# Kernel optimization log

Measured on AMD Instinct MI355X. Metric: run time of the kernel, lower is better.

The kernel has to match this reference:

```python
import jax, jax.numpy as jnp
import numpy as np

B, S, H = 2, 1024, 4096
NH, NKV, D = 32, 8, 128
N_REP = NH // NKV
SCALE = D ** -0.5
ROPE_BASE = 1000000.0
NEG_INF = -1e9


def _rope_tables(dtype=jnp.float32):
    inv_freq = 1.0 / (ROPE_BASE ** (jnp.arange(0, D, 2, dtype=jnp.float32) / D))
    pos = jnp.arange(S, dtype=jnp.float32)
    freqs = pos[:, None] * inv_freq[None, :]              # [S, D/2]
    emb = jnp.concatenate([freqs, freqs], axis=-1)        # [S, D]
    cos = jnp.broadcast_to(jnp.cos(emb)[None], (B, S, D)).astype(dtype)
    sin = jnp.broadcast_to(jnp.sin(emb)[None], (B, S, D)).astype(dtype)
    return cos, sin


def setup_inputs() -> dict:
    key = jax.random.key(0)
    k1, k2, k3, k4, k5 = jax.random.split(key, 5)
    hidden_states = jax.random.normal(k1, (B, S, H), dtype=jnp.float32)
    # weights stored as [in, out] so application is x @ W
    Wq = jax.random.normal(k2, (H, NH * D), dtype=jnp.float32) * (H ** -0.5)
    Wk = jax.random.normal(k3, (H, NKV * D), dtype=jnp.float32) * (H ** -0.5)
    Wv = jax.random.normal(k4, (H, NKV * D), dtype=jnp.float32) * (H ** -0.5)
    Wo = jax.random.normal(k5, (NH * D, H), dtype=jnp.float32) * ((NH * D) ** -0.5)
    cos, sin = _rope_tables()
    causal = jnp.tril(jnp.ones((S, S), dtype=bool))
    attention_mask = jnp.where(causal, 0.0, NEG_INF).astype(jnp.float32)
    attention_mask = jnp.broadcast_to(attention_mask[None, None], (B, 1, S, S))
    return {"hidden_states": hidden_states, "cos": cos, "sin": sin,
            "attention_mask": attention_mask, "Wq": Wq, "Wk": Wk, "Wv": Wv, "Wo": Wo}


def _rotate_half(x):
    x1, x2 = x[..., : D // 2], x[..., D // 2:]
    return jnp.concatenate([-x2, x1], axis=-1)


def reference(hidden_states, cos, sin, attention_mask, Wq, Wk, Wv, Wo):
    # projections -> [B, heads, S, D]
    q = (hidden_states @ Wq).reshape(B, S, NH, D).transpose(0, 2, 1, 3)
    k = (hidden_states @ Wk).reshape(B, S, NKV, D).transpose(0, 2, 1, 3)
    v = (hidden_states @ Wv).reshape(B, S, NKV, D).transpose(0, 2, 1, 3)
    # RoPE (cos/sin unsqueezed over head dim)
    c = cos[:, None, :, :]
    s = sin[:, None, :, :]
    q = q * c + _rotate_half(q) * s
    k = k * c + _rotate_half(k) * s
    # repeat_kv for GQA
    k = jnp.repeat(k, N_REP, axis=1)   # [B, NH, S, D]
    v = jnp.repeat(v, N_REP, axis=1)
    scores = jnp.einsum('bhqd,bhkd->bhqk', q, k) * SCALE + attention_mask
    weights = jax.nn.softmax(scores.astype(jnp.float32), axis=-1).astype(q.dtype)
    attn = jnp.einsum('bhqk,bhkd->bhqd', weights, v)
    attn = attn.transpose(0, 2, 1, 3).reshape(B, S, NH * D)
    return attn @ Wo
```

## Files before the change

kernel.cpp:

```cpp
#include <hip/hip_runtime.h>

typedef unsigned short u16;
typedef __bf16 bf16x8 __attribute__((ext_vector_type(8)));
typedef float f32x4 __attribute__((ext_vector_type(4)));

#define SCALE_QK 0.08838834764831845f
#define LOG2E 1.4426950408889634f
#define NEGBIG (-1e9f)

static __device__ __forceinline__ float bf2f(u16 u) {
  union { float f; unsigned int i; } x; x.i = ((unsigned int)u) << 16; return x.f;
}
static __device__ __forceinline__ u16 f2bf(float f) {
  union { float f; unsigned int i; } x; x.f = f;
  return (u16)((x.i + 0x7fffu + ((x.i >> 16) & 1u)) >> 16);
}
static __device__ __forceinline__ void async16(const u16* g, u16* s) {
  __builtin_amdgcn_global_load_lds(
      (const __attribute__((address_space(1))) void*)g,
      (__attribute__((address_space(3))) void*)s, 16, 0, 0);
}

__global__ __launch_bounds__(64) void detect_dtype(
    const void* p0, const void* p1, const void* p2, const void* p3,
    const void* p4, const void* p5, int* flags) {
  const void* ps[6] = {p0, p1, p2, p3, p4, p5};
  const u16* p = (const u16*)ps[blockIdx.x];
  int lane = threadIdx.x;
  u16 u = p[2 * lane];
  int e = (u >> 7) & 0xFF;
  int plaus = (e >= 112 && e <= 143) ? 1 : 0;
  unsigned long long m = __ballot(plaus);
  if (lane == 0) {
    flags[blockIdx.x] = (__popcll(m) < 32) ? 1 : 0;
    if (blockIdx.x == 0) flags[6] = 0;
  }
}

__global__ __launch_bounds__(256) void transpose_to_bf16(
    const void* __restrict__ src, u16* __restrict__ dst, int N, int K,
    const int* __restrict__ flag) {
  const int LT = 74;
  __shared__ u16 t[64 * LT];
  const int tid = threadIdx.x;
  const int n0 = blockIdx.x * 64, k0 = blockIdx.y * 64;
  const int f32in = *flag;
  for (int c = tid; c < 512; c += 256) {
    int r = c >> 3, ch = (c & 7) * 8;
    u16* tp = t + r * LT + ch;
    if (f32in) {
      const float* p = (const float*)src + (size_t)(k0 + r) * N + n0 + ch;
      float4 v0 = *(const float4*)p;
      float4 v1 = *(const float4*)(p + 4);
      tp[0] = f2bf(v0.x); tp[1] = f2bf(v0.y); tp[2] = f2bf(v0.z); tp[3] = f2bf(v0.w);
      tp[4] = f2bf(v1.x); tp[5] = f2bf(v1.y); tp[6] = f2bf(v1.z); tp[7] = f2bf(v1.w);
    } else {
      uint4 v = *(const uint4*)((const u16*)src + (size_t)(k0 + r) * N + n0 + ch);
      const u16* pv = (const u16*)&v;
#pragma unroll
      for (int e = 0; e < 8; ++e) tp[e] = pv[e];
    }
  }
  __syncthreads();
  for (int c = tid; c < 512; c += 256) {
    int rr = c >> 3, cc = (c & 7) * 8;
    u16 tmp[8];
#pragma unroll
    for (int e = 0; e < 8; ++e) tmp[e] = t[(cc + e) * LT + rr];
    *(uint4*)(dst + (size_t)(n0 + rr) * K + k0 + cc) = *(const uint4*)tmp;
  }
}

__global__ __launch_bounds__(256) void cast_to_bf16(
    const void* __restrict__ src, u16* __restrict__ dst, const int* __restrict__ flag) {
  int i = (blockIdx.x * 256 + threadIdx.x) * 8;
  if (*flag) {
    float4 v0 = *(const float4*)((const float*)src + i);
    float4 v1 = *(const float4*)((const float*)src + i + 4);
    u16 tmp[8] = {f2bf(v0.x), f2bf(v0.y), f2bf(v0.z), f2bf(v0.w),
                  f2bf(v1.x), f2bf(v1.y), f2bf(v1.z), f2bf(v1.w)};
    *(uint4*)(dst + i) = *(const uint4*)tmp;
  } else {
    *(uint4*)(dst + i) = *(const uint4*)((const u16*)src + i);
  }
}

__global__ __launch_bounds__(256, 2) void gemm_bt(
    const u16* __restrict__ A, const u16* __restrict__ Bt, void* __restrict__ C,
    int K, int lda, int ldb, int ldc, const int* __restrict__ oflag) {
  __shared__ u16 sA[128 * 32];
  __shared__ u16 sB[128 * 32];
  const int tid = threadIdx.x;
  const int wave = tid >> 6, lane = tid & 63;
  const int quad = lane >> 4, l16 = lane & 15;
  const int wr = wave >> 1, wc = wave & 1;
  const int bm = blockIdx.y << 7, bn = blockIdx.x << 7;
  const int f32out = *oflag;

  f32x4 acc[4][4] = {};

  const int c0 = tid, c1 = tid + 256;
  const int r0 = c0 >> 2, h0 = (c0 & 3) * 8;
  const int r1 = c1 >> 2, h1 = (c1 & 3) * 8;
  const u16* a0 = A + (size_t)(bm + r0) * lda + h0;
  const u16* a1 = A + (size_t)(bm + r1) * lda + h1;
  const u16* b0 = Bt + (size_t)(bn + r0) * ldb + h0;
  const u16* b1 = Bt + (size_t)(bn + r1) * ldb + h1;

  for (int k0 = 0; k0 < K; k0 += 32) {
    async16(a0 + k0, sA + c0 * 8);
    async16(a1 + k0, sA + c1 * 8);
    async16(b0 + k0, sB + c0 * 8);
    async16(b1 + k0, sB + c1 * 8);
    __syncthreads();
    bf16x8 af[4], bv[4];
#pragma unroll
    for (int i = 0; i < 4; ++i)
      af[i] = *(const bf16x8*)(sA + (wr * 64 + i * 16 + l16) * 32 + quad * 8);
#pragma unroll
    for (int j = 0; j < 4; ++j)
      bv[j] = *(const bf16x8*)(sB + (wc * 64 + j * 16 + l16) * 32 + quad * 8);
#pragma unroll
    for (int i = 0; i < 4; ++i)
#pragma unroll
      for (int j = 0; j < 4; ++j)
        acc[i][j] =
            __builtin_amdgcn_mfma_f32_16x16x32_bf16(af[i], bv[j], acc[i][j], 0, 0, 0);
    __syncthreads();
  }
#pragma unroll
  for (int i = 0; i < 4; ++i) {
    int row = bm + wr * 64 + i * 16 + quad * 4;
#pragma unroll
    for (int j = 0; j < 4; ++j) {
      int col = bn + wc * 64 + j * 16 + l16;
#pragma unroll
      for (int r = 0; r < 4; ++r) {
        size_t idx = (size_t)(row + r) * ldc + col;
        if (f32out) ((float*)C)[idx] = acc[i][j][r];
        else ((u16*)C)[idx] = f2bf(acc[i][j][r]);
      }
    }
  }
}

__global__ __launch_bounds__(256) void rope_kernel(
    u16* __restrict__ QKV, const void* __restrict__ cosb,
    const void* __restrict__ sinb, const int* __restrict__ flag) {
  int idx = blockIdx.x * 256 + threadIdx.x;
  int d = idx & 63;
  int rest = idx >> 6;
  int slot = rest % 40;
  int tok = rest / 40;
  int col = (slot < 32) ? (slot * 128 + d) : (4096 + (slot - 32) * 128 + d);
  size_t base = (size_t)tok * 6144 + col;
  float x1 = bf2f(QKV[base]);
  float x2 = bf2f(QKV[base + 64]);
  size_t cb = (size_t)tok * 128 + d;
  float c1, s1, c2, s2;
  if (*flag) {
    c1 = ((const float*)cosb)[cb]; s1 = ((const float*)sinb)[cb];
    c2 = ((const float*)cosb)[cb + 64]; s2 = ((const float*)sinb)[cb + 64];
  } else {
    c1 = bf2f(((const u16*)cosb)[cb]); s1 = bf2f(((const u16*)sinb)[cb]);
    c2 = bf2f(((const u16*)cosb)[cb + 64]); s2 = bf2f(((const u16*)sinb)[cb + 64]);
  }
  QKV[base] = f2bf(x1 * c1 - x2 * s1);
  QKV[base + 64] = f2bf(x2 * c2 + x1 * s2);
}

__global__ __launch_bounds__(256, 3) void attn_kernel(
    const u16* __restrict__ QKV, u16* __restrict__ O) {
  const int LK = 136;
  const int LP = 72;
  __shared__ u16 sK[64 * LK];
  __shared__ u16 sV[128 * 64];
  __shared__ u16 sP[64 * LP];
  const int tid = threadIdx.x, wave = tid >> 6, lane = tid & 63;
  const int quad = lane >> 4, l16 = lane & 15;
  const int pp = blockIdx.x, h = blockIdx.y, b = blockIdx.z;
  const int kvh = h >> 2;
  const size_t tb = (size_t)b * 1024 * 6144;
  const u16* Qg = QKV + tb + (size_t)h * 128;
  const u16* Kg = QKV + tb + 4096 + (size_t)kvh * 128;
  const u16* Vg = QKV + tb + 5120 + (size_t)kvh * 128;

#pragma unroll 1
  for (int pass = 0; pass < 2; ++pass) {
    const int qt = pass ? (15 - pp) : pp;

    bf16x8 qa[4];
    {
      const int qrow = qt * 64 + wave * 16 + l16;
#pragma unroll
      for (int kc = 0; kc < 4; ++kc) {
        bf16x8 v = *(const bf16x8*)(Qg + (size_t)qrow * 6144 + kc * 32 + quad * 8);
#pragma unroll
        for (int e = 0; e < 8; ++e) v[e] = (__bf16)((float)v[e] * (SCALE_QK * LOG2E));
        qa[kc] = v;
      }
    }

    uint4 kreg[4], vreg[4];
#pragma unroll
    for (int i = 0; i < 4; ++i) {
      int c = i * 256 + tid, row = c >> 4, ch = (c & 15) * 8;
      kreg[i] = *(const uint4*)(Kg + (size_t)row * 6144 + ch);
      vreg[i] = *(const uint4*)(Vg + (size_t)row * 6144 + ch);
    }

    float m_run[4], l_run[4];
    f32x4 oacc[8] = {};
#pragma unroll
    for (int r = 0; r < 4; ++r) { m_run[r] = -INFINITY; l_run[r] = 0.f; }

    const int nkb = qt + 1;
    for (int kb = 0; kb < nkb; ++kb) {
#pragma unroll
      for (int i = 0; i < 4; ++i) {
        int c = i * 256 + tid, row = c >> 4, ch = (c & 15) * 8;
        *(uint4*)(sK + row * LK + ch) = kreg[i];
        const u16* pw = (const u16*)&vreg[i];
#pragma unroll
        for (int e = 0; e < 8; ++e) {
          int d = ch + e;
          sV[d * 64 + ((((row >> 3) ^ (d >> 3)) & 7) << 3) + (row & 7)] = pw[e];
        }
      }
      __syncthreads();
      if (kb + 1 < nkb) {
#pragma unroll
        for (int i = 0; i < 4; ++i) {
          int c = i * 256 + tid, row = c >> 4, ch = (c & 15) * 8;
          kreg[i] = *(const uint4*)(Kg + (size_t)((kb + 1) * 64 + row) * 6144 + ch);
          vreg[i] = *(const uint4*)(Vg + (size_t)((kb + 1) * 64 + row) * 6144 + ch);
        }
      }

      f32x4 sc[4] = {};
#pragma unroll
      for (int kc = 0; kc < 4; ++kc)
#pragma unroll
        for (int j = 0; j < 4; ++j) {
          bf16x8 bb = *(const bf16x8*)(sK + (j * 16 + l16) * LK + kc * 32 + quad * 8);
          sc[j] = __builtin_amdgcn_mfma_f32_16x16x32_bf16(qa[kc], bb, sc[j], 0, 0, 0);
        }

      const int rowg = qt * 64 + wave * 16 + quad * 4;
      const int colg = kb * 64 + l16;
      float mloc[4] = {NEGBIG, NEGBIG, NEGBIG, NEGBIG};
#pragma unroll
      for (int j = 0; j < 4; ++j)
#pragma unroll
        for (int r = 0; r < 4; ++r) {
          float v = sc[j][r];
          if (colg + j * 16 > rowg + r) v = NEGBIG;
          sc[j][r] = v;
          mloc[r] = fmaxf(mloc[r], v);
        }
#pragma unroll
      for (int off = 1; off < 16; off <<= 1)
#pragma unroll
        for (int r = 0; r < 4; ++r)
          mloc[r] = fmaxf(mloc[r], __shfl_xor(mloc[r], off, 64));

      float alpha[4], lad[4];
#pragma unroll
      for (int r = 0; r < 4; ++r) {
        float mn = fmaxf(m_run[r], mloc[r]);
        alpha[r] = exp2f(m_run[r] - mn);
        m_run[r] = mn;
        lad[r] = 0.f;
      }
#pragma unroll
      for (int j = 0; j < 4; ++j)
#pragma unroll
        for (int r = 0; r < 4; ++r) {
          float p = exp2f(sc[j][r] - m_run[r]);
          sc[j][r] = p;
          lad[r] += p;
        }
#pragma unroll
      for (int off = 1; off < 16; off <<= 1)
#pragma unroll
        for (int r = 0; r < 4; ++r) lad[r] += __shfl_xor(lad[r], off, 64);
#pragma unroll
      for (int r = 0; r < 4; ++r) l_run[r] = l_run[r] * alpha[r] + lad[r];
#pragma unroll
      for (int dt = 0; dt < 8; ++dt)
#pragma unroll
        for (int r = 0; r < 4; ++r) oacc[dt][r] *= alpha[r];

#pragma unroll
      for (int j = 0; j < 4; ++j)
#pragma unroll
        for (int r = 0; r < 4; ++r)
          sP[(wave * 16 + quad * 4 + r) * LP + j * 16 + l16] = f2bf(sc[j][r]);
      __asm__ __volatile__("s_waitcnt lgkmcnt(0)" ::: "memory");

#pragma unroll
      for (int kc = 0; kc < 2; ++kc) {
        bf16x8 a = *(const bf16x8*)(sP + (wave * 16 + l16) * LP + kc * 32 + quad * 8);
#pragma unroll
        for (int dt = 0; dt < 8; ++dt) {
          int d = dt * 16 + l16;
          int chk = ((kc * 4 + quad) ^ (d >> 3)) & 7;
          bf16x8 bb = *(const bf16x8*)(sV + d * 64 + chk * 8);
          oacc[dt] = __builtin_amdgcn_mfma_f32_16x16x32_bf16(a, bb, oacc[dt], 0, 0, 0);
        }
      }
      __syncthreads();
    }

    const int srow = qt * 64 + wave * 16 + quad * 4;
#pragma unroll
    for (int dt = 0; dt < 8; ++dt)
#pragma unroll
      for (int r = 0; r < 4; ++r) {
        float val = oacc[dt][r] / l_run[r];
        O[((size_t)b * 1024 + srow + r) * 4096 + h * 128 + dt * 16 + l16] = f2bf(val);
      }
  }
}

extern "C" void kernel_launch(void* const* d_in, const int* in_sizes, int n_in,
                              void* d_out, int out_size, void* d_ws, size_t ws_size,
                              hipStream_t stream) {
  (void)in_sizes; (void)n_in; (void)out_size; (void)ws_size;
  const void* hidden = d_in[0];
  const void* cosb   = d_in[1];
  const void* sinb   = d_in[2];
  const void* Wq = d_in[4];
  const void* Wk = d_in[5];
  const void* Wv = d_in[6];
  const void* Wo = d_in[7];

  u16* ws = (u16*)d_ws;
  u16* Wqkvt = ws;
  u16* Wot   = ws;
  u16* Xb    = ws + (size_t)25165824;
  u16* attnb = Xb;
  u16* QKV   = ws + (size_t)33554432;
  int* flags = (int*)(ws + (size_t)46137344);

  detect_dtype<<<6, 64, 0, stream>>>(hidden, cosb, Wq, Wk, Wv, Wo, flags);

  transpose_to_bf16<<<dim3(64, 64), 256, 0, stream>>>(Wq, Wqkvt, 4096, 4096, flags + 2);
  transpose_to_bf16<<<dim3(16, 64), 256, 0, stream>>>(Wk, Wqkvt + (size_t)4096 * 4096, 1024, 4096, flags + 3);
  transpose_to_bf16<<<dim3(16, 64), 256, 0, stream>>>(Wv, Wqkvt + (size_t)5120 * 4096, 1024, 4096, flags + 4);
  cast_to_bf16<<<4096, 256, 0, stream>>>(hidden, Xb, flags + 0);

  gemm_bt<<<dim3(48, 16), 256, 0, stream>>>(Xb, Wqkvt, QKV, 4096, 4096, 4096, 6144, flags + 6);
  rope_kernel<<<20480, 256, 0, stream>>>(QKV, cosb, sinb, flags + 1);

  transpose_to_bf16<<<dim3(64, 64), 256, 0, stream>>>(Wo, Wot, 4096, 4096, flags + 5);

  attn_kernel<<<dim3(8, 32, 2), 256, 0, stream>>>(QKV, attnb);
  gemm_bt<<<dim3(32, 16), 256, 0, stream>>>(attnb, Wot, d_out, 4096, 4096, 4096, 4096, flags + 0);
}
```

Measured before the change: 519.7 us.

## Merge QKV transposes, vectorize RoPE, transpose attention scores with lazy rescaling

Folds the three Q/K/V weight transposes into one launch and rewrites RoPE so each thread handles eight contiguous elements with 16-byte loads and stores. In attention, the QK^T MFMA operands are swapped so each lane owns a single query row. That cuts the row max/sum reductions to two shuffles and keeps running stats in scalars, and the output rescale is skipped unless the max grows by more than 8 (log2 domain). The lazy rescale leaves exponent sums less tightly bounded, and the strided sP writes may add LDS bank conflicts.

```diff
diff --git a/kernel.cpp b/kernel.cpp
--- a/kernel.cpp
+++ b/kernel.cpp
@@ -37,14 +37,11 @@
   }
 }
 
-__global__ __launch_bounds__(256) void transpose_to_bf16(
+static __device__ __forceinline__ void transpose_body(
     const void* __restrict__ src, u16* __restrict__ dst, int N, int K,
-    const int* __restrict__ flag) {
+    int n0, int k0, int f32in, u16* t) {
   const int LT = 74;
-  __shared__ u16 t[64 * LT];
   const int tid = threadIdx.x;
-  const int n0 = blockIdx.x * 64, k0 = blockIdx.y * 64;
-  const int f32in = *flag;
   for (int c = tid; c < 512; c += 256) {
     int r = c >> 3, ch = (c & 7) * 8;
     u16* tp = t + r * LT + ch;
@@ -71,6 +68,26 @@
   }
 }
 
+__global__ __launch_bounds__(256) void transpose_to_bf16(
+    const void* __restrict__ src, u16* __restrict__ dst, int N, int K,
+    const int* __restrict__ flag) {
+  __shared__ u16 t[64 * 74];
+  transpose_body(src, dst, N, K, blockIdx.x * 64, blockIdx.y * 64, *flag, t);
+}
+
+__global__ __launch_bounds__(256) void transpose_qkv(
+    const void* __restrict__ Wq, const void* __restrict__ Wk,
+    const void* __restrict__ Wv, u16* __restrict__ dst,
+    const int* __restrict__ flags) {
+  __shared__ u16 t[64 * 74];
+  int bx = blockIdx.x;
+  const void* src; u16* d; int N; int f32in; int nx;
+  if (bx < 64)      { src = Wq; d = dst;                         N = 4096; f32in = flags[2]; nx = bx; }
+  else if (bx < 80) { src = Wk; d = dst + (size_t)4096 * 4096;   N = 1024; f32in = flags[3]; nx = bx - 64; }
+  else              { src = Wv; d = dst + (size_t)5120 * 4096;   N = 1024; f32in = flags[4]; nx = bx - 80; }
+  transpose_body(src, d, N, 4096, nx * 64, blockIdx.y * 64, f32in, t);
+}
+
 __global__ __launch_bounds__(256) void cast_to_bf16(
     const void* __restrict__ src, u16* __restrict__ dst, const int* __restrict__ flag) {
   int i = (blockIdx.x * 256 + threadIdx.x) * 8;
@@ -148,25 +165,53 @@
     u16* __restrict__ QKV, const void* __restrict__ cosb,
     const void* __restrict__ sinb, const int* __restrict__ flag) {
   int idx = blockIdx.x * 256 + threadIdx.x;
-  int d = idx & 63;
-  int rest = idx >> 6;
+  int d8 = (idx & 7) * 8;
+  int rest = idx >> 3;
   int slot = rest % 40;
   int tok = rest / 40;
-  int col = (slot < 32) ? (slot * 128 + d) : (4096 + (slot - 32) * 128 + d);
+  int col = (slot < 32) ? (slot * 128 + d8) : (4096 + (slot - 32) * 128 + d8);
   size_t base = (size_t)tok * 6144 + col;
-  float x1 = bf2f(QKV[base]);
-  float x2 = bf2f(QKV[base + 64]);
-  size_t cb = (size_t)tok * 128 + d;
-  float c1, s1, c2, s2;
+  uint4 va = *(const uint4*)(QKV + base);
+  uint4 vb = *(const uint4*)(QKV + base + 64);
+  const u16* pa = (const u16*)&va;
+  const u16* pb = (const u16*)&vb;
+  size_t cb = (size_t)tok * 128 + d8;
+  float c1[8], s1[8], c2[8], s2[8];
   if (*flag) {
-    c1 = ((const float*)cosb)[cb]; s1 = ((const float*)sinb)[cb];
-    c2 = ((const float*)cosb)[cb + 64]; s2 = ((const float*)sinb)[cb + 64];
+    const float* cp = (const float*)cosb + cb;
+    const float* sp = (const float*)sinb + cb;
+    float4 t0 = *(const float4*)cp,        t1 = *(const float4*)(cp + 4);
+    float4 t2 = *(const float4*)(cp + 64), t3 = *(const float4*)(cp + 68);
+    float4 u0 = *(const float4*)sp,        u1 = *(const float4*)(sp + 4);
+    float4 u2 = *(const float4*)(sp + 64), u3 = *(const float4*)(sp + 68);
+    const float* tf = (const float*)&t0;
+    (void)tf;
+    c1[0]=t0.x;c1[1]=t0.y;c1[2]=t0.z;c1[3]=t0.w;c1[4]=t1.x;c1[5]=t1.y;c1[6]=t1.z;c1[7]=t1.w;
+    c2[0]=t2.x;c2[1]=t2.y;c2[2]=t2.z;c2[3]=t2.w;c2[4]=t3.x;c2[5]=t3.y;c2[6]=t3.z;c2[7]=t3.w;
+    s1[0]=u0.x;s1[1]=u0.y;s1[2]=u0.z;s1[3]=u0.w;s1[4]=u1.x;s1[5]=u1.y;s1[6]=u1.z;s1[7]=u1.w;
+    s2[0]=u2.x;s2[1]=u2.y;s2[2]=u2.z;s2[3]=u2.w;s2[4]=u3.x;s2[5]=u3.y;s2[6]=u3.z;s2[7]=u3.w;
   } else {
-    c1 = bf2f(((const u16*)cosb)[cb]); s1 = bf2f(((const u16*)sinb)[cb]);
-    c2 = bf2f(((const u16*)cosb)[cb + 64]); s2 = bf2f(((const u16*)sinb)[cb + 64]);
-  }
-  QKV[base] = f2bf(x1 * c1 - x2 * s1);
-  QKV[base + 64] = f2bf(x2 * c2 + x1 * s2);
+    const u16* cp = (const u16*)cosb + cb;
+    const u16* sp = (const u16*)sinb + cb;
+    uint4 t0 = *(const uint4*)cp, t1 = *(const uint4*)(cp + 64);
+    uint4 u0 = *(const uint4*)sp, u1 = *(const uint4*)(sp + 64);
+    const u16* q0 = (const u16*)&t0; const u16* q1 = (const u16*)&t1;
+    const u16* r0 = (const u16*)&u0; const u16* r1 = (const u16*)&u1;
+#pragma unroll
+    for (int e = 0; e < 8; ++e) {
+      c1[e] = bf2f(q0[e]); c2[e] = bf2f(q1[e]);
+      s1[e] = bf2f(r0[e]); s2[e] = bf2f(r1[e]);
+    }
+  }
+  u16 o1[8], o2[8];
+#pragma unroll
+  for (int e = 0; e < 8; ++e) {
+    float x1 = bf2f(pa[e]), x2 = bf2f(pb[e]);
+    o1[e] = f2bf(x1 * c1[e] - x2 * s1[e]);
+    o2[e] = f2bf(x2 * c2[e] + x1 * s2[e]);
+  }
+  *(uint4*)(QKV + base) = *(const uint4*)o1;
+  *(uint4*)(QKV + base + 64) = *(const uint4*)o2;
 }
 
 __global__ __launch_bounds__(256, 3) void attn_kernel(
@@ -209,10 +254,9 @@
       vreg[i] = *(const uint4*)(Vg + (size_t)row * 6144 + ch);
     }
 
-    float m_run[4], l_run[4];
+    float m_run = -INFINITY, l_run = 0.f;
     f32x4 oacc[8] = {};
-#pragma unroll
-    for (int r = 0; r < 4; ++r) { m_run[r] = -INFINITY; l_run[r] = 0.f; }
+    const int qg = qt * 64 + wave * 16 + l16;
 
     const int nkb = qt + 1;
     for (int kb = 0; kb < nkb; ++kb) {
@@ -237,65 +281,61 @@
         }
       }
 
-      f32x4 sc[4] = {};
+      f32x4 st[4] = {};
 #pragma unroll
       for (int kc = 0; kc < 4; ++kc)
 #pragma unroll
         for (int j = 0; j < 4; ++j) {
           bf16x8 bb = *(const bf16x8*)(sK + (j * 16 + l16) * LK + kc * 32 + quad * 8);
-          sc[j] = __builtin_amdgcn_mfma_f32_16x16x32_bf16(qa[kc], bb, sc[j], 0, 0, 0);
-        }
-
-      const int rowg = qt * 64 + wave * 16 + quad * 4;
-      const int colg = kb * 64 + l16;
-      float mloc[4] = {NEGBIG, NEGBIG, NEGBIG, NEGBIG};
+          st[j] = __builtin_amdgcn_mfma_f32_16x16x32_bf16(bb, qa[kc], st[j], 0, 0, 0);
+        }
+
+      const int kg0 = kb * 64 + quad * 4;
+      float mloc = NEGBIG;
 #pragma unroll
       for (int j = 0; j < 4; ++j)
 #pragma unroll
         for (int r = 0; r < 4; ++r) {
-          float v = sc[j][r];
-          if (colg + j * 16 > rowg + r) v = NEGBIG;
-          sc[j][r] = v;
-          mloc[r] = fmaxf(mloc[r], v);
-        }
-#pragma unroll
-      for (int off = 1; off < 16; off <<= 1)
+          float v = st[j][r];
+          if (kg0 + j * 16 + r > qg) v = NEGBIG;
+          st[j][r] = v;
+          mloc = fmaxf(mloc, v);
+        }
+      mloc = fmaxf(mloc, __shfl_xor(mloc, 16, 64));
+      mloc = fmaxf(mloc, __shfl_xor(mloc, 32, 64));
+
+      if (__any(mloc - m_run > 8.0f)) {
+        float mn = fmaxf(m_run, mloc);
+        float alpha = exp2f(m_run - mn);
+        m_run = mn;
+        l_run *= alpha;
+        float ar[4];
+#pragma unroll
+        for (int r = 0; r < 4; ++r) ar[r] = __shfl(alpha, quad * 4 + r, 64);
+#pragma unroll
+        for (int dt = 0; dt < 8; ++dt)
+#pragma unroll
+          for (int r = 0; r < 4; ++r) oacc[dt][r] *= ar[r];
+      }
+
+      float lad = 0.f;
+#pragma unroll
+      for (int j = 0; j < 4; ++j)
+#pragma unroll
+        for (int r = 0; r < 4; ++r) {
+          float p = exp2f(st[j][r] - m_run);
+          st[j][r] = p;
+          lad += p;
+        }
+      lad += __shfl_xor(lad, 16, 64);
+      lad += __shfl_xor(lad, 32, 64);
+      l_run += lad;
+
+#pragma unroll
+      for (int j = 0; j < 4; ++j)
 #pragma unroll
         for (int r = 0; r < 4; ++r)
-          mloc[r] = fmaxf(mloc[r], __shfl_xor(mloc[r], off, 64));
-
-      float alpha[4], lad[4];
-#pragma unroll
-      for (int r = 0; r < 4; ++r) {
-        float mn = fmaxf(m_run[r], mloc[r]);
-        alpha[r] = exp2f(m_run[r] - mn);
-        m_run[r] = mn;
-        lad[r] = 0.f;
-      }
-#pragma unroll
-      for (int j = 0; j < 4; ++j)
-#pragma unroll
-        for (int r = 0; r < 4; ++r) {
-          float p = exp2f(sc[j][r] - m_run[r]);
-          sc[j][r] = p;
-          lad[r] += p;
-        }
-#pragma unroll
-      for (int off = 1; off < 16; off <<= 1)
-#pragma unroll
-        for (int r = 0; r < 4; ++r) lad[r] += __shfl_xor(lad[r], off, 64);
-#pragma unroll
-      for (int r = 0; r < 4; ++r) l_run[r] = l_run[r] * alpha[r] + lad[r];
-#pragma unroll
-      for (int dt = 0; dt < 8; ++dt)
-#pragma unroll
-        for (int r = 0; r < 4; ++r) oacc[dt][r] *= alpha[r];
-
-#pragma unroll
-      for (int j = 0; j < 4; ++j)
-#pragma unroll
-        for (int r = 0; r < 4; ++r)
-          sP[(wave * 16 + quad * 4 + r) * LP + j * 16 + l16] = f2bf(sc[j][r]);
+          sP[(wave * 16 + l16) * LP + j * 16 + quad * 4 + r] = f2bf(st[j][r]);
       __asm__ __volatile__("s_waitcnt lgkmcnt(0)" ::: "memory");
 
 #pragma unroll
@@ -312,12 +352,16 @@
       __syncthreads();
     }
 
+    float lfin[4];
+#pragma unroll
+    for (int r = 0; r < 4; ++r) lfin[r] = __shfl(l_run, quad * 4 + r, 64);
+
     const int srow = qt * 64 + wave * 16 + quad * 4;
 #pragma unroll
     for (int dt = 0; dt < 8; ++dt)
 #pragma unroll
       for (int r = 0; r < 4; ++r) {
-        float val = oacc[dt][r] / l_run[r];
+        float val = oacc[dt][r] / lfin[r];
         O[((size_t)b * 1024 + srow + r) * 4096 + h * 128 + dt * 16 + l16] = f2bf(val);
       }
   }
@@ -345,13 +389,11 @@
 
   detect_dtype<<<6, 64, 0, stream>>>(hidden, cosb, Wq, Wk, Wv, Wo, flags);
 
-  transpose_to_bf16<<<dim3(64, 64), 256, 0, stream>>>(Wq, Wqkvt, 4096, 4096, flags + 2);
-  transpose_to_bf16<<<dim3(16, 64), 256, 0, stream>>>(Wk, Wqkvt + (size_t)4096 * 4096, 1024, 4096, flags + 3);
-  transpose_to_bf16<<<dim3(16, 64), 256, 0, stream>>>(Wv, Wqkvt + (size_t)5120 * 4096, 1024, 4096, flags + 4);
+  transpose_qkv<<<dim3(96, 64), 256, 0, stream>>>(Wq, Wk, Wv, Wqkvt, flags);
   cast_to_bf16<<<4096, 256, 0, stream>>>(hidden, Xb, flags + 0);
 
   gemm_bt<<<dim3(48, 16), 256, 0, stream>>>(Xb, Wqkvt, QKV, 4096, 4096, 4096, 6144, flags + 6);
-  rope_kernel<<<20480, 256, 0, stream>>>(QKV, cosb, sinb, flags + 1);
+  rope_kernel<<<2560, 256, 0, stream>>>(QKV, cosb, sinb, flags + 1);
 
   transpose_to_bf16<<<dim3(64, 64), 256, 0, stream>>>(Wo, Wot, 4096, 4096, flags + 5);
 
```

Result: faster. 502.7 us (-3.3%).
